# Performance work log

Measured on AMD Instinct MI355X. Metric: run time of the kernel, lower is better.

The kernel has to match this reference:

```python
import jax, jax.numpy as jnp
import numpy as np
import math
from jax import lax

B, T, IN_DIM, D, H, L, OUT = 2, 2048, 128, 512, 8, 4, 128
HD = D // H
FF = int(4.0 * D)
NEG = -1e30  # stands in for -inf in the causal mask (identical softmax result)


def setup_inputs() -> dict:
    key = jax.random.key(0)
    ks = jax.random.split(key, 8)
    s = 0.02
    def p(k, shape):
        return jax.random.normal(k, shape, jnp.float32) * s
    return {
        "x": jax.random.normal(ks[0], (B, T, IN_DIM), jnp.float32),
        "Win": p(ks[1], (IN_DIM, D)), "bin_": jnp.zeros((D,), jnp.float32),
        "Wqkv": p(ks[2], (L, D, 3 * D)), "bqkv": jnp.zeros((L, 3 * D), jnp.float32),
        "Wo": p(ks[3], (L, D, D)), "bo": jnp.zeros((L, D), jnp.float32),
        "ln1_g": jnp.ones((L, D), jnp.float32), "ln1_b": jnp.zeros((L, D), jnp.float32),
        "Wf1": p(ks[4], (L, D, FF)), "bf1": jnp.zeros((L, FF), jnp.float32),
        "Wf2": p(ks[5], (L, FF, D)), "bf2": jnp.zeros((L, D), jnp.float32),
        "ln2_g": jnp.ones((L, D), jnp.float32), "ln2_b": jnp.zeros((L, D), jnp.float32),
        "lnf_g": jnp.ones((D,), jnp.float32), "lnf_b": jnp.zeros((D,), jnp.float32),
        "Wout": p(ks[6], (D, OUT)), "bout": jnp.zeros((OUT,), jnp.float32),
    }


def _layernorm(x, g, b, eps=1e-5):
    mu = jnp.mean(x, axis=-1, keepdims=True)
    var = jnp.mean(jnp.square(x - mu), axis=-1, keepdims=True)
    return (x - mu) * lax.rsqrt(var + eps) * g + b


def _sinusoidal_pe(t, d):
    pos = jnp.arange(t, dtype=jnp.float32)[:, None]
    div = jnp.exp(jnp.arange(0, d, 2, dtype=jnp.float32) * (-math.log(10000.0) / d))
    pe = jnp.zeros((t, d), jnp.float32)
    pe = pe.at[:, 0::2].set(jnp.sin(pos * div)).at[:, 1::2].set(jnp.cos(pos * div))
    return pe


def _alibi_bias():
    # ALiBi slopes (H=8 is a power of 2): start = 2**(-2**(-(log2(H)-3)))
    start = 2.0 ** (-(2.0 ** (-(math.log2(H) - 3.0))))
    slopes = jnp.array([start * (start ** i) for i in range(H)], jnp.float32)
    pos = jnp.arange(T)
    dist = jnp.triu(pos[None, :] - pos[:, None]).astype(jnp.float32)  # faithful: .triu() zeroes j<i
    bias = slopes[:, None, None] * dist  # [H,T,T]
    causal = jnp.triu(jnp.ones((T, T), bool), 1)
    return jnp.where(causal[None], NEG, bias)


def _forward(x, Win, bin_, Wqkv, bqkv, Wo, bo, ln1_g, ln1_b, Wf1, bf1, Wf2, bf2,
             ln2_g, ln2_b, lnf_g, lnf_b, Wout, bout):
    x = x @ Win + bin_                      # [B,T,D] project_in
    x = x + _sinusoidal_pe(T, D)            # internal time embedding
    bias = _alibi_bias()                    # [H,T,T]
    scale = 1.0 / math.sqrt(HD)

    def block(h, params):
        wqkv, bq, wo, bo_, g1, b1, wf1, bf1_, wf2, bf2_, g2, b2 = params
        y = _layernorm(h, g1, b1)
        qkv = y @ wqkv + bq                 # [B,T,3D]
        q, k, v = jnp.split(qkv, 3, axis=-1)
        def heads(t):
            return t.reshape(B, T, H, HD).transpose(0, 2, 1, 3)  # [B,H,T,HD]
        q, k, v = heads(q), heads(k), heads(v)
        logits = jnp.einsum('bhqd,bhkd->bhqk', q, k) * scale + bias[None]
        attn = jax.nn.softmax(logits, axis=-1)
        y = jnp.einsum('bhqk,bhkd->bhqd', attn, v)
        y = y.transpose(0, 2, 1, 3).reshape(B, T, D)
        h = h + (y @ wo + bo_)
        y = _layernorm(h, g2, b2)
        y = jax.nn.gelu(y @ wf1 + bf1_, approximate=False) @ wf2 + bf2_
        h = h + y
        return h, None

    x, _ = lax.scan(block, x, (Wqkv, bqkv, Wo, bo, ln1_g, ln1_b, Wf1, bf1, Wf2, bf2, ln2_g, ln2_b))
    x = _layernorm(x, lnf_g, lnf_b)         # final_norm
    return x @ Wout + bout                  # output head


def reference(x, Win, bin_, Wqkv, bqkv, Wo, bo, ln1_g, ln1_b, Wf1, bf1, Wf2, bf2,
              ln2_g, ln2_b, lnf_g, lnf_b, Wout, bout):
    return _forward(x, Win, bin_, Wqkv, bqkv, Wo, bo, ln1_g, ln1_b, Wf1, bf1,
                    Wf2, bf2, ln2_g, ln2_b, lnf_g, lnf_b, Wout, bout)
```

## Files before the change

kernel.cpp:

```cpp
#include <hip/hip_runtime.h>
#include <math.h>
#include <type_traits>
#include <utility>

#define TT 2048
typedef unsigned short u16;
typedef unsigned int u32;
typedef float f32x4 __attribute__((ext_vector_type(4)));
typedef float f32x16 __attribute__((ext_vector_type(16)));
typedef short s16x8 __attribute__((ext_vector_type(8)));
typedef __bf16 bf16x8 __attribute__((ext_vector_type(8)));
typedef __bf16 bf16x2 __attribute__((ext_vector_type(2)));
typedef u32 u32x4 __attribute__((ext_vector_type(4)));

enum { EPI_PE = 0, EPI_QKV = 1, EPI_RES = 2, EPI_GELU = 3, EPI_OUTF = 4 };

template<typename V, typename = void> struct mfma_takes : std::false_type {};
template<typename V> struct mfma_takes<V, std::void_t<decltype(
    __builtin_amdgcn_mfma_f32_16x16x32_bf16(std::declval<V>(), std::declval<V>(),
                                            std::declval<f32x4>(), 0, 0, 0))>>
    : std::true_type {};

template<typename VA>
__device__ __forceinline__ f32x4 MFMA_t(VA a, VA b, f32x4 c) {
    if constexpr (mfma_takes<VA>::value) {
        return __builtin_amdgcn_mfma_f32_16x16x32_bf16(a, b, c, 0, 0, 0);
    } else {
        return __builtin_amdgcn_mfma_f32_16x16x32_bf16(
            __builtin_bit_cast(bf16x8, a), __builtin_bit_cast(bf16x8, b), c, 0, 0, 0);
    }
}

template<typename V, typename = void> struct mfma32_takes : std::false_type {};
template<typename V> struct mfma32_takes<V, std::void_t<decltype(
    __builtin_amdgcn_mfma_f32_32x32x16_bf16(std::declval<V>(), std::declval<V>(),
                                            std::declval<f32x16>(), 0, 0, 0))>>
    : std::true_type {};

template<typename VA>
__device__ __forceinline__ f32x16 MFMA32(VA a, VA b, f32x16 c) {
    if constexpr (mfma32_takes<VA>::value) {
        return __builtin_amdgcn_mfma_f32_32x32x16_bf16(a, b, c, 0, 0, 0);
    } else {
        return __builtin_amdgcn_mfma_f32_32x32x16_bf16(
            __builtin_bit_cast(bf16x8, a), __builtin_bit_cast(bf16x8, b), c, 0, 0, 0);
    }
}

__device__ __forceinline__ u16 f2b(float f) {
    u32 u = __float_as_uint(f);
    return (u16)((u + 0x7FFFu + ((u >> 16) & 1u)) >> 16);
}

__device__ __forceinline__ u32 pkbf(float a, float b) {
    bf16x2 t; t[0] = (__bf16)a; t[1] = (__bf16)b;
    return __builtin_bit_cast(u32, t);
}

__device__ __forceinline__ void gload16(const void* g, void* lds_base, int lds_byte_off) {
    __builtin_amdgcn_global_load_lds(
        (const __attribute__((address_space(1))) void*)g,
        (__attribute__((address_space(3))) void*)((char*)lds_base + lds_byte_off),
        16, 0, 0);
}

template<int EPI, int TM, int TN>
__global__ __launch_bounds__(256)
void k_gemm_mfma(const u16* __restrict__ A, const u16* __restrict__ Bt,
                 const float* __restrict__ bias, const float* __restrict__ Rf,
                 void* __restrict__ Cout, u16* __restrict__ Kfp,
                 u16* __restrict__ Vfp, int M, int N, int K)
{
    constexpr int MF = TM / 32;
    constexpr int NF = TN / 32;
    __shared__ __attribute__((aligned(16))) u16 SMEM[TM * 64 + TN * 64];
    u16* As = SMEM;
    u16* Bs = SMEM + TM * 64;
    const int tid = threadIdx.x;
    const int l = tid & 63, wv = tid >> 6;
    const int l15 = l & 15, lg = l >> 4;
    const int wr = wv >> 1, wc = wv & 1;
    const int row0 = blockIdx.y * TM, col0 = blockIdx.x * TN;

    f32x4 acc[MF][NF];
#pragma unroll
    for (int m = 0; m < MF; ++m)
#pragma unroll
        for (int n = 0; n < NF; ++n) acc[m][n] = (f32x4){0.f, 0.f, 0.f, 0.f};

    for (int kt = 0; kt < K; kt += 64) {
#pragma unroll
        for (int i = 0; i < TM / 32; ++i) {
            const int u = i * 256 + wv * 64 + l;
            const int ar = u >> 3, ac = u & 7;
            const int sc = (ac ^ (ar & 7)) << 3;
            const int off = __builtin_amdgcn_readfirstlane((i * 256 + wv * 64) * 16);
            gload16(A + (size_t)(row0 + ar) * K + kt + sc, As, off);
        }
#pragma unroll
        for (int i = 0; i < TN / 32; ++i) {
            const int u = i * 256 + wv * 64 + l;
            const int ar = u >> 3, ac = u & 7;
            const int sc = (ac ^ (ar & 7)) << 3;
            const int off = __builtin_amdgcn_readfirstlane((i * 256 + wv * 64) * 16);
            gload16(Bt + (size_t)(col0 + ar) * K + kt + sc, Bs, off);
        }
        __syncthreads();
        s16x8 af[MF][2], bf[NF][2];
#pragma unroll
        for (int m = 0; m < MF; ++m) {
            const int r = wr * (TM / 2) + m * 16 + l15;
#pragma unroll
            for (int s = 0; s < 2; ++s)
                af[m][s] = *(const s16x8*)(As + r * 64 + (((s * 4 + lg) ^ (r & 7)) << 3));
        }
#pragma unroll
        for (int n = 0; n < NF; ++n) {
            const int r = wc * (TN / 2) + n * 16 + l15;
#pragma unroll
            for (int s = 0; s < 2; ++s)
                bf[n][s] = *(const s16x8*)(Bs + r * 64 + (((s * 4 + lg) ^ (r & 7)) << 3));
        }
#pragma unroll
        for (int s = 0; s < 2; ++s)
#pragma unroll
            for (int m = 0; m < MF; ++m)
#pragma unroll
                for (int n = 0; n < NF; ++n)
                    acc[m][n] = MFMA_t(af[m][s], bf[n][s], acc[m][n]);
        __syncthreads();
    }

    if constexpr (EPI == EPI_QKV) {
        if (col0 < 512) {
#pragma unroll
            for (int m = 0; m < MF; ++m)
#pragma unroll
                for (int rg = 0; rg < 4; ++rg) {
                    const int row = row0 + wr * (TM / 2) + m * 16 + lg * 4 + rg;
#pragma unroll
                    for (int n = 0; n < NF; ++n) {
                        const int col = col0 + wc * (TN / 2) + n * 16 + l15;
                        ((u16*)Cout)[(size_t)row * N + col] = f2b(acc[m][n][rg] + bias[col]);
                    }
                }
        } else if (col0 < 1024) {
#pragma unroll
            for (int m = 0; m < MF; ++m)
#pragma unroll
                for (int rg = 0; rg < 4; ++rg) {
                    const int row = row0 + wr * (TM / 2) + m * 16 + lg * 4 + rg;
                    const int t = row & (TT - 1), bb = row >> 11;
#pragma unroll
                    for (int n = 0; n < NF; ++n) {
                        const int col = col0 + wc * (TN / 2) + n * 16 + l15;
                        const int dd = col - 512;
                        const int hh = dd >> 6, c = (dd >> 3) & 7, j = dd & 7;
                        Kfp[(((size_t)(bb * 8 + hh) * 8 + c) * 2048 + t) * 8 + j]
                            = f2b(acc[m][n][rg] + bias[col]);
                    }
                }
        } else {
            u16* TV = SMEM;
#pragma unroll
            for (int m = 0; m < MF; ++m)
#pragma unroll
                for (int rg = 0; rg < 4; ++rg) {
                    const int rr = wr * (TM / 2) + m * 16 + lg * 4 + rg;
#pragma unroll
                    for (int n = 0; n < NF; ++n) {
                        const int cc_ = wc * (TN / 2) + n * 16 + l15;
                        TV[rr * 128 + cc_] = f2b(acc[m][n][rg] + bias[col0 + cc_]);
                    }
                }
            __syncthreads();
            const int gt = (row0 & (TT - 1)) >> 6, bb = row0 >> 11;
            const int hh0 = (col0 - 1024) >> 6;
#pragma unroll
            for (int i = 0; i < 4; ++i) {
                const int u = i * 256 + tid;
                const int hsel = u >> 9, rem = u & 511;
                const int cc = rem >> 6, d = rem & 63;
                u32 pk[4];
#pragma unroll
                for (int jp = 0; jp < 4; ++jp)
                    pk[jp] = (u32)TV[(cc * 8 + 2 * jp) * 128 + hsel * 64 + d]
                           | ((u32)TV[(cc * 8 + 2 * jp + 1) * 128 + hsel * 64 + d] << 16);
                *(uint4*)(Vfp + ((((size_t)(bb * 8 + hh0 + hsel) * 32 + gt) * 8 + cc) * 64 + d) * 8)
                    = make_uint4(pk[0], pk[1], pk[2], pk[3]);
            }
        }
        return;
    }

#pragma unroll
    for (int m = 0; m < MF; ++m)
#pragma unroll
        for (int rg = 0; rg < 4; ++rg) {
            const int row = row0 + wr * (TM / 2) + m * 16 + lg * 4 + rg;
#pragma unroll
            for (int n = 0; n < NF; ++n) {
                const int col = col0 + wc * (TN / 2) + n * 16 + l15;
                float v = acc[m][n][rg] + bias[col];
                const size_t idx = (size_t)row * N + col;
                if constexpr (EPI == EPI_PE) {
                    const int t = row & (TT - 1);
                    const float freq = __expf(-(float)(col & ~1) * 0.017988946039015984f);
                    const float ang = (float)t * freq;
                    v += (col & 1) ? cosf(ang) : sinf(ang);
                    ((float*)Cout)[idx] = v;
                } else if constexpr (EPI == EPI_GELU) {
                    v = 0.5f * v * (1.f + erff(v * 0.7071067811865475f));
                    ((u16*)Cout)[idx] = f2b(v);
                } else if constexpr (EPI == EPI_RES) {
                    ((float*)Cout)[idx] = Rf[idx] + v;
                } else {
                    ((float*)Cout)[idx] = v;
                }
            }
        }
}

__global__ __launch_bounds__(256)
void k_ln(const float* __restrict__ X, const float* __restrict__ g,
          const float* __restrict__ b, u16* __restrict__ Y)
{
    const int lane = threadIdx.x & 63;
    const int row = blockIdx.x * 4 + (threadIdx.x >> 6);
    const float* x = X + (size_t)row * 512 + lane * 8;

    float4 v0 = *(const float4*)x;
    float4 v1 = *(const float4*)(x + 4);
    float vals[8] = {v0.x, v0.y, v0.z, v0.w, v1.x, v1.y, v1.z, v1.w};

    float s = 0.f;
#pragma unroll
    for (int i = 0; i < 8; ++i) s += vals[i];
#pragma unroll
    for (int off = 32; off >= 1; off >>= 1) s += __shfl_xor(s, off);
    const float mu = s * (1.f / 512.f);

    float sq = 0.f;
#pragma unroll
    for (int i = 0; i < 8; ++i) { float d = vals[i] - mu; sq += d * d; }
#pragma unroll
    for (int off = 32; off >= 1; off >>= 1) sq += __shfl_xor(sq, off);
    const float rs = rsqrtf(sq * (1.f / 512.f) + 1e-5f);

    const float* gp = g + lane * 8;
    const float* bp = b + lane * 8;
    float4 g0 = *(const float4*)gp, g1 = *(const float4*)(gp + 4);
    float4 b0 = *(const float4*)bp, b1 = *(const float4*)(bp + 4);
    float ga[8] = {g0.x, g0.y, g0.z, g0.w, g1.x, g1.y, g1.z, g1.w};
    float bb[8] = {b0.x, b0.y, b0.z, b0.w, b1.x, b1.y, b1.z, b1.w};

    u32 pk[4];
#pragma unroll
    for (int i = 0; i < 4; ++i) {
        float a0 = (vals[2 * i]     - mu) * rs * ga[2 * i]     + bb[2 * i];
        float a1 = (vals[2 * i + 1] - mu) * rs * ga[2 * i + 1] + bb[2 * i + 1];
        pk[i] = (u32)f2b(a0) | ((u32)f2b(a1) << 16);
    }
    *(uint4*)(Y + (size_t)row * 512 + lane * 8) = make_uint4(pk[0], pk[1], pk[2], pk[3]);
}

__global__ __launch_bounds__(256, 4)
void k_attn(const u16* __restrict__ qkv, const u16* __restrict__ Kf,
            const u16* __restrict__ Vf, u16* __restrict__ y)
{
    __shared__ float Om[4][32 * 65];
    __shared__ float Ml[4][32][2];
    const int tid = threadIdx.x;
    const int l = tid & 63, w = tid >> 6;
    const int l31 = l & 31, hi = l >> 5;
    const int bx = blockIdx.x;
    const int xcd = bx & 7, s = bx >> 3;
    const int bh = xcd * 2 + (s & 1);
    const int t_tile = 63 - (s >> 1);
    const int b = bh >> 3, hh = bh & 7;
    const int bT = b * TT, hh64 = hh * 64;

    const int qg = t_tile * 32 + l31;
    const int NT = (t_tile >> 1) + 1;

    f32x16 o[2] = {};
    float m = -1e30f, lsum = 0.f;

    if (w < NT) {
        s16x8 qf[4];
        {
            const u16* qsrc = qkv + (size_t)(bT + qg) * 1536 + hh64 + hi * 8;
#pragma unroll
            for (int dk = 0; dk < 4; ++dk) qf[dk] = *(const s16x8*)(qsrc + dk * 16);
        }
        const u16* kfb = Kf + ((size_t)bh * 8 + hi) * 2048 * 8;
        const u16* vfb = Vf + (((size_t)bh * 32) * 8 + hi) * 64 * 8;

        for (int g = w; g < NT; g += 4) {
            s16x8 kf[8];
#pragma unroll
            for (int nb = 0; nb < 2; ++nb)
#pragma unroll
                for (int dk = 0; dk < 4; ++dk)
                    kf[nb * 4 + dk] = *(const s16x8*)(
                        kfb + ((size_t)(dk * 2) * 2048 + g * 64 + nb * 32 + l31) * 8);

            f32x16 sA[2];
#pragma unroll
            for (int nb = 0; nb < 2; ++nb) {
                f32x16 acc = {};
#pragma unroll
                for (int dk = 0; dk < 4; ++dk) acc = MFMA32(kf[nb * 4 + dk], qf[dk], acc);
                sA[nb] = acc;
            }

            if (g == NT - 1) {
                const int kvb = g * 64, hi4 = hi * 4;
#pragma unroll
                for (int nb = 0; nb < 2; ++nb)
#pragma unroll
                    for (int r = 0; r < 16; ++r) {
                        const int kv = kvb + nb * 32 + (r & 3) + 8 * (r >> 2) + hi4;
                        sA[nb][r] = (kv > qg) ? -1e30f : sA[nb][r];
                    }
            }

            float tmp[16];
#pragma unroll
            for (int r = 0; r < 16; ++r) tmp[r] = fmaxf(sA[0][r], sA[1][r]);
#pragma unroll
            for (int st = 8; st >= 1; st >>= 1)
#pragma unroll
                for (int r = 0; r < 8; ++r)
                    if (r < st) tmp[r] = fmaxf(tmp[r], tmp[r + st]);
            float mt = fmaxf(tmp[0], __shfl_xor(tmp[0], 32));
            const bool grow = !__all(mt <= m);
            if (grow) {
                const float mn = fmaxf(m, mt);
                const float alpha = __expf((m - mn) * 0.125f);
                m = mn;
                lsum *= alpha;
#pragma unroll
                for (int dt = 0; dt < 2; ++dt)
#pragma unroll
                    for (int r = 0; r < 16; ++r) o[dt][r] *= alpha;
            }
            const float mc = -m * 0.125f;

            float p[2][16];
            float sum[16];
#pragma unroll
            for (int r = 0; r < 16; ++r) {
                p[0][r] = __expf(fmaf(sA[0][r], 0.125f, mc));
                p[1][r] = __expf(fmaf(sA[1][r], 0.125f, mc));
                sum[r] = p[0][r] + p[1][r];
            }
#pragma unroll
            for (int st = 8; st >= 1; st >>= 1)
#pragma unroll
                for (int r = 0; r < 8; ++r)
                    if (r < st) sum[r] += sum[r + st];
            float psum = sum[0] + __shfl_xor(sum[0], 32);
            lsum += psum;

            u32 pk2[2][8], sw2[2][8];
#pragma unroll
            for (int nb = 0; nb < 2; ++nb)
#pragma unroll
                for (int i = 0; i < 8; ++i) {
                    pk2[nb][i] = pkbf(p[nb][2 * i], p[nb][2 * i + 1]);
                    sw2[nb][i] = __shfl_xor(pk2[nb][i], 32);
                }
            s16x8 pa[4];
#pragma unroll
            for (int nb = 0; nb < 2; ++nb)
#pragma unroll
                for (int k16 = 0; k16 < 2; ++k16) {
                    const int i0 = k16 * 4;
                    u32 w0 = hi ? sw2[nb][i0 + 2] : pk2[nb][i0 + 0];
                    u32 w1 = hi ? sw2[nb][i0 + 3] : pk2[nb][i0 + 1];
                    u32 w2 = hi ? pk2[nb][i0 + 2] : sw2[nb][i0 + 0];
                    u32 w3 = hi ? pk2[nb][i0 + 3] : sw2[nb][i0 + 1];
                    u32x4 t4 = {w0, w1, w2, w3};
                    pa[nb * 2 + k16] = __builtin_bit_cast(s16x8, t4);
                }

#pragma unroll
            for (int dt = 0; dt < 2; ++dt) {
                f32x16 acc = o[dt];
#pragma unroll
                for (int ks = 0; ks < 4; ++ks)
                    acc = MFMA32(*(const s16x8*)(
                        vfb + (((size_t)g * 8 + ks * 2) * 64 + dt * 32 + l31) * 8),
                        pa[ks], acc);
                o[dt] = acc;
            }
        }
    }

#pragma unroll
    for (int dt = 0; dt < 2; ++dt)
#pragma unroll
        for (int r = 0; r < 16; ++r) {
            const int d = dt * 32 + (r & 3) + 8 * (r >> 2) + 4 * hi;
            Om[w][l31 * 65 + d] = o[dt][r];
        }
    Ml[w][l31][0] = m;
    Ml[w][l31][1] = lsum;
    __syncthreads();

    const int q = tid & 31, d0 = (tid >> 5) * 8;
    float m0 = Ml[0][q][0], m1 = Ml[1][q][0], m2 = Ml[2][q][0], m3 = Ml[3][q][0];
    const float mstar = fmaxf(fmaxf(m0, m1), fmaxf(m2, m3));
    float sc[4];
    sc[0] = __expf((m0 - mstar) * 0.125f);
    sc[1] = __expf((m1 - mstar) * 0.125f);
    sc[2] = __expf((m2 - mstar) * 0.125f);
    sc[3] = __expf((m3 - mstar) * 0.125f);
    const float lstar = sc[0] * Ml[0][q][1] + sc[1] * Ml[1][q][1]
                      + sc[2] * Ml[2][q][1] + sc[3] * Ml[3][q][1];
    float ov[8];
#pragma unroll
    for (int j = 0; j < 8; ++j) ov[j] = 0.f;
#pragma unroll
    for (int ww = 0; ww < 4; ++ww) {
        const float scw = sc[ww];
        const float* src = &Om[ww][q * 65 + d0];
#pragma unroll
        for (int j = 0; j < 8; ++j) ov[j] = fmaf(scw, src[j], ov[j]);
    }
    const float inv = 1.f / lstar;
    u32 pk[4];
#pragma unroll
    for (int i = 0; i < 4; ++i) pk[i] = pkbf(ov[2 * i] * inv, ov[2 * i + 1] * inv);
    u16* yp = y + (size_t)(bT + t_tile * 32 + q) * 512 + hh64 + d0;
    *(uint4*)yp = make_uint4(pk[0], pk[1], pk[2], pk[3]);
}

__global__ __launch_bounds__(256)
void k_wt_all(const float* __restrict__ Wqkv, const float* __restrict__ Wo,
              const float* __restrict__ Wf1, const float* __restrict__ Wf2,
              const float* __restrict__ Win, const float* __restrict__ Wout,
              u16* __restrict__ WqkvT, u16* __restrict__ WoT,
              u16* __restrict__ Wf1T, u16* __restrict__ Wf2T,
              u16* __restrict__ WinT, u16* __restrict__ WoutT)
{
    __shared__ float T[64][65];
    const int tid = threadIdx.x;
    int id = blockIdx.x;
    const float* W; u16* Wt; int K, N;
    if (id < 3072) {
        const int lyr = id / 768, sub = id - lyr * 768;
        if (sub < 192)      { W = Wqkv + (size_t)lyr * 512 * 1536; Wt = WqkvT + (size_t)lyr * 512 * 1536; K = 512;  N = 1536; id = sub; }
        else if (sub < 256) { W = Wo   + (size_t)lyr * 512 * 512;  Wt = WoT   + (size_t)lyr * 512 * 512;  K = 512;  N = 512;  id = sub - 192; }
        else if (sub < 512) { W = Wf1  + (size_t)lyr * 512 * 2048; Wt = Wf1T  + (size_t)lyr * 512 * 2048; K = 512;  N = 2048; id = sub - 256; }
        else                { W = Wf2  + (size_t)lyr * 2048 * 512; Wt = Wf2T  + (size_t)lyr * 2048 * 512; K = 2048; N = 512;  id = sub - 512; }
    } else if (id < 3088)   { W = Win;  Wt = WinT;  K = 128; N = 512; id -= 3072; }
    else                    { W = Wout; Wt = WoutT; K = 512; N = 128; id -= 3088; }
    const int nt = N >> 6;
    const int ktile = id / nt, ntile = id - ktile * nt;
    const int kb = ktile * 64, nb = ntile * 64;
#pragma unroll
    for (int i = 0; i < 4; ++i) {
        const int r = i * 16 + (tid >> 4), c = (tid & 15) * 4;
        const float4 v = *(const float4*)&W[(size_t)(kb + r) * N + nb + c];
        T[r][c] = v.x; T[r][c + 1] = v.y; T[r][c + 2] = v.z; T[r][c + 3] = v.w;
    }
    __syncthreads();
    const int n = tid >> 2, k0 = (tid & 3) * 16;
    u32 pk[8];
#pragma unroll
    for (int i = 0; i < 8; ++i)
        pk[i] = pkbf(T[k0 + 2 * i][n], T[k0 + 2 * i + 1][n]);
    uint4* dst = (uint4*)(Wt + (size_t)(nb + n) * K + kb + k0);
    dst[0] = make_uint4(pk[0], pk[1], pk[2], pk[3]);
    dst[1] = make_uint4(pk[4], pk[5], pk[6], pk[7]);
}

__global__ __launch_bounds__(256)
void k_f2b(const float* __restrict__ x, u16* __restrict__ xb)
{
    const int g = blockIdx.x * 256 + threadIdx.x;
    const float4* s = (const float4*)(x + (size_t)g * 8);
    float4 a = s[0], c = s[1];
    u32 pk[4] = {
        (u32)f2b(a.x) | ((u32)f2b(a.y) << 16), (u32)f2b(a.z) | ((u32)f2b(a.w) << 16),
        (u32)f2b(c.x) | ((u32)f2b(c.y) << 16), (u32)f2b(c.z) | ((u32)f2b(c.w) << 16)};
    *(uint4*)(xb + (size_t)g * 8) = make_uint4(pk[0], pk[1], pk[2], pk[3]);
}

extern "C" void kernel_launch(void* const* d_in, const int* in_sizes, int n_in,
                              void* d_out, int out_size, void* d_ws, size_t ws_size,
                              hipStream_t stream)
{
    const float* x    = (const float*)d_in[0];
    const float* Win  = (const float*)d_in[1];
    const float* bin_ = (const float*)d_in[2];
    const float* Wqkv = (const float*)d_in[3];
    const float* bqkv = (const float*)d_in[4];
    const float* Wo   = (const float*)d_in[5];
    const float* bo   = (const float*)d_in[6];
    const float* ln1g = (const float*)d_in[7];
    const float* ln1b = (const float*)d_in[8];
    const float* Wf1  = (const float*)d_in[9];
    const float* bf1  = (const float*)d_in[10];
    const float* Wf2  = (const float*)d_in[11];
    const float* bf2  = (const float*)d_in[12];
    const float* ln2g = (const float*)d_in[13];
    const float* ln2b = (const float*)d_in[14];
    const float* lnfg = (const float*)d_in[15];
    const float* lnfb = (const float*)d_in[16];
    const float* Wout = (const float*)d_in[17];
    const float* bout = (const float*)d_in[18];
    float* out = (float*)d_out;

    const int M = 4096;
    char* ws = (char*)d_ws;
    float* h    = (float*)(ws + 0);
    u16*   y    = (u16*)(ws + 8388608);
    u16*   big  = (u16*)(ws + 12582912);
    u16*   Kf   = (u16*)(ws + 29360128);
    u16*   Vf   = (u16*)(ws + 33554432);
    u16*   xb   = big;
    u16*   WinT  = (u16*)(ws + 37748736);
    u16*   WoutT = (u16*)(ws + 37879808);
    u16*   WqkvT = (u16*)(ws + 38010880);
    u16*   WoT   = (u16*)(ws + 44302336);
    u16*   Wf1T  = (u16*)(ws + 46399488);
    u16*   Wf2T  = (u16*)(ws + 54788096);

    dim3 blk(256);

    k_f2b<<<256, blk, 0, stream>>>(x, xb);
    k_wt_all<<<3104, blk, 0, stream>>>(Wqkv, Wo, Wf1, Wf2, Win, Wout,
                                       WqkvT, WoT, Wf1T, Wf2T, WinT, WoutT);

    k_gemm_mfma<EPI_PE, 64, 64><<<dim3(8, 64), blk, 0, stream>>>(
        xb, WinT, bin_, nullptr, h, nullptr, nullptr, M, 512, 128);

    for (int lyr = 0; lyr < 4; ++lyr) {
        k_ln<<<1024, blk, 0, stream>>>(h, ln1g + lyr * 512, ln1b + lyr * 512, y);
        k_gemm_mfma<EPI_QKV, 64, 128><<<dim3(12, 64), blk, 0, stream>>>(
            y, WqkvT + (size_t)lyr * 512 * 1536, bqkv + lyr * 1536, nullptr,
            big, Kf, Vf, M, 1536, 512);
        k_attn<<<1024, blk, 0, stream>>>(big, Kf, Vf, y);
        k_gemm_mfma<EPI_RES, 64, 64><<<dim3(8, 64), blk, 0, stream>>>(
            y, WoT + (size_t)lyr * 512 * 512, bo + lyr * 512, h, h, nullptr, nullptr, M, 512, 512);
        k_ln<<<1024, blk, 0, stream>>>(h, ln2g + lyr * 512, ln2b + lyr * 512, y);
        k_gemm_mfma<EPI_GELU, 64, 128><<<dim3(16, 64), blk, 0, stream>>>(
            y, Wf1T + (size_t)lyr * 512 * 2048, bf1 + lyr * 2048, nullptr,
            big, nullptr, nullptr, M, 2048, 512);
        k_gemm_mfma<EPI_RES, 64, 64><<<dim3(8, 64), blk, 0, stream>>>(
            big, Wf2T + (size_t)lyr * 2048 * 512, bf2 + lyr * 512, h, h, nullptr, nullptr, M, 512, 2048);
    }

    k_ln<<<1024, blk, 0, stream>>>(h, lnfg, lnfb, y);
    k_gemm_mfma<EPI_OUTF, 64, 64><<<dim3(2, 64), blk, 0, stream>>>(
        y, WoutT, bout, nullptr, out, nullptr, nullptr, M, 128, 512);
}
```

Measured before the change: 468.9 us.

## Switch GEMM to 32x32 MFMA, use exp2 in softmax, add setprio around MFMAs

The GEMM kernel now issues 32x32x16 bf16 MFMA instead of 16x16x32. Each wave computes 32-row fragments and reads four k-slices per 64-wide tile, and all epilogues are remapped to the 32x32 output layout. The attention kernel replaces __expf with the native exp2 by folding log2(e)/8 into the scale. It also raises wave priority around its MFMA blocks to favour matrix issue. This cuts operand-load and instruction overhead and exp cost, but it needs tiles that are multiples of 64 per wave and a correct remap of the output layout.

```diff
diff --git a/kernel.cpp b/kernel.cpp
--- a/kernel.cpp
+++ b/kernel.cpp
@@ -13,23 +13,10 @@
 typedef __bf16 bf16x2 __attribute__((ext_vector_type(2)));
 typedef u32 u32x4 __attribute__((ext_vector_type(4)));
 
+#define L2E8 0.1803368801111731f
+#define EXP2(x) __builtin_amdgcn_exp2f(x)
+
 enum { EPI_PE = 0, EPI_QKV = 1, EPI_RES = 2, EPI_GELU = 3, EPI_OUTF = 4 };
-
-template<typename V, typename = void> struct mfma_takes : std::false_type {};
-template<typename V> struct mfma_takes<V, std::void_t<decltype(
-    __builtin_amdgcn_mfma_f32_16x16x32_bf16(std::declval<V>(), std::declval<V>(),
-                                            std::declval<f32x4>(), 0, 0, 0))>>
-    : std::true_type {};
-
-template<typename VA>
-__device__ __forceinline__ f32x4 MFMA_t(VA a, VA b, f32x4 c) {
-    if constexpr (mfma_takes<VA>::value) {
-        return __builtin_amdgcn_mfma_f32_16x16x32_bf16(a, b, c, 0, 0, 0);
-    } else {
-        return __builtin_amdgcn_mfma_f32_16x16x32_bf16(
-            __builtin_bit_cast(bf16x8, a), __builtin_bit_cast(bf16x8, b), c, 0, 0, 0);
-    }
-}
 
 template<typename V, typename = void> struct mfma32_takes : std::false_type {};
 template<typename V> struct mfma32_takes<V, std::void_t<decltype(
@@ -71,22 +58,18 @@
                  void* __restrict__ Cout, u16* __restrict__ Kfp,
                  u16* __restrict__ Vfp, int M, int N, int K)
 {
-    constexpr int MF = TM / 32;
-    constexpr int NF = TN / 32;
+    constexpr int MF = TM / 64;
+    constexpr int NF = TN / 64;
     __shared__ __attribute__((aligned(16))) u16 SMEM[TM * 64 + TN * 64];
     u16* As = SMEM;
     u16* Bs = SMEM + TM * 64;
     const int tid = threadIdx.x;
     const int l = tid & 63, wv = tid >> 6;
-    const int l15 = l & 15, lg = l >> 4;
+    const int l31 = l & 31, hi = l >> 5;
     const int wr = wv >> 1, wc = wv & 1;
     const int row0 = blockIdx.y * TM, col0 = blockIdx.x * TN;
 
-    f32x4 acc[MF][NF];
-#pragma unroll
-    for (int m = 0; m < MF; ++m)
-#pragma unroll
-        for (int n = 0; n < NF; ++n) acc[m][n] = (f32x4){0.f, 0.f, 0.f, 0.f};
+    f32x16 acc[MF][NF] = {};
 
     for (int kt = 0; kt < K; kt += 64) {
 #pragma unroll
@@ -106,28 +89,28 @@
             gload16(Bt + (size_t)(col0 + ar) * K + kt + sc, Bs, off);
         }
         __syncthreads();
-        s16x8 af[MF][2], bf[NF][2];
+        s16x8 af[MF][4], bf[NF][4];
 #pragma unroll
         for (int m = 0; m < MF; ++m) {
-            const int r = wr * (TM / 2) + m * 16 + l15;
-#pragma unroll
-            for (int s = 0; s < 2; ++s)
-                af[m][s] = *(const s16x8*)(As + r * 64 + (((s * 4 + lg) ^ (r & 7)) << 3));
+            const int r = wr * (TM / 2) + m * 32 + l31;
+#pragma unroll
+            for (int kk = 0; kk < 4; ++kk)
+                af[m][kk] = *(const s16x8*)(As + r * 64 + (((kk * 2 + hi) ^ (r & 7)) << 3));
         }
 #pragma unroll
         for (int n = 0; n < NF; ++n) {
-            const int r = wc * (TN / 2) + n * 16 + l15;
-#pragma unroll
-            for (int s = 0; s < 2; ++s)
-                bf[n][s] = *(const s16x8*)(Bs + r * 64 + (((s * 4 + lg) ^ (r & 7)) << 3));
-        }
-#pragma unroll
-        for (int s = 0; s < 2; ++s)
+            const int r = wc * (TN / 2) + n * 32 + l31;
+#pragma unroll
+            for (int kk = 0; kk < 4; ++kk)
+                bf[n][kk] = *(const s16x8*)(Bs + r * 64 + (((kk * 2 + hi) ^ (r & 7)) << 3));
+        }
+#pragma unroll
+        for (int kk = 0; kk < 4; ++kk)
 #pragma unroll
             for (int m = 0; m < MF; ++m)
 #pragma unroll
                 for (int n = 0; n < NF; ++n)
-                    acc[m][n] = MFMA_t(af[m][s], bf[n][s], acc[m][n]);
+                    acc[m][n] = MFMA32(af[m][kk], bf[n][kk], acc[m][n]);
         __syncthreads();
     }
 
@@ -136,28 +119,28 @@
 #pragma unroll
             for (int m = 0; m < MF; ++m)
 #pragma unroll
-                for (int rg = 0; rg < 4; ++rg) {
-                    const int row = row0 + wr * (TM / 2) + m * 16 + lg * 4 + rg;
+                for (int r = 0; r < 16; ++r) {
+                    const int row = row0 + wr * (TM / 2) + m * 32 + (r & 3) + 8 * (r >> 2) + 4 * hi;
 #pragma unroll
                     for (int n = 0; n < NF; ++n) {
-                        const int col = col0 + wc * (TN / 2) + n * 16 + l15;
-                        ((u16*)Cout)[(size_t)row * N + col] = f2b(acc[m][n][rg] + bias[col]);
+                        const int col = col0 + wc * (TN / 2) + n * 32 + l31;
+                        ((u16*)Cout)[(size_t)row * N + col] = f2b(acc[m][n][r] + bias[col]);
                     }
                 }
         } else if (col0 < 1024) {
 #pragma unroll
             for (int m = 0; m < MF; ++m)
 #pragma unroll
-                for (int rg = 0; rg < 4; ++rg) {
-                    const int row = row0 + wr * (TM / 2) + m * 16 + lg * 4 + rg;
+                for (int r = 0; r < 16; ++r) {
+                    const int row = row0 + wr * (TM / 2) + m * 32 + (r & 3) + 8 * (r >> 2) + 4 * hi;
                     const int t = row & (TT - 1), bb = row >> 11;
 #pragma unroll
                     for (int n = 0; n < NF; ++n) {
-                        const int col = col0 + wc * (TN / 2) + n * 16 + l15;
+                        const int col = col0 + wc * (TN / 2) + n * 32 + l31;
                         const int dd = col - 512;
                         const int hh = dd >> 6, c = (dd >> 3) & 7, j = dd & 7;
                         Kfp[(((size_t)(bb * 8 + hh) * 8 + c) * 2048 + t) * 8 + j]
-                            = f2b(acc[m][n][rg] + bias[col]);
+                            = f2b(acc[m][n][r] + bias[col]);
                     }
                 }
         } else {
@@ -165,12 +148,12 @@
 #pragma unroll
             for (int m = 0; m < MF; ++m)
 #pragma unroll
-                for (int rg = 0; rg < 4; ++rg) {
-                    const int rr = wr * (TM / 2) + m * 16 + lg * 4 + rg;
+                for (int r = 0; r < 16; ++r) {
+                    const int rr = wr * (TM / 2) + m * 32 + (r & 3) + 8 * (r >> 2) + 4 * hi;
 #pragma unroll
                     for (int n = 0; n < NF; ++n) {
-                        const int cc_ = wc * (TN / 2) + n * 16 + l15;
-                        TV[rr * 128 + cc_] = f2b(acc[m][n][rg] + bias[col0 + cc_]);
+                        const int cc_ = wc * (TN / 2) + n * 32 + l31;
+                        TV[rr * 128 + cc_] = f2b(acc[m][n][r] + bias[col0 + cc_]);
                     }
                 }
             __syncthreads();
@@ -196,12 +179,12 @@
 #pragma unroll
     for (int m = 0; m < MF; ++m)
 #pragma unroll
-        for (int rg = 0; rg < 4; ++rg) {
-            const int row = row0 + wr * (TM / 2) + m * 16 + lg * 4 + rg;
+        for (int r = 0; r < 16; ++r) {
+            const int row = row0 + wr * (TM / 2) + m * 32 + (r & 3) + 8 * (r >> 2) + 4 * hi;
 #pragma unroll
             for (int n = 0; n < NF; ++n) {
-                const int col = col0 + wc * (TN / 2) + n * 16 + l15;
-                float v = acc[m][n][rg] + bias[col];
+                const int col = col0 + wc * (TN / 2) + n * 32 + l31;
+                float v = acc[m][n][r] + bias[col];
                 const size_t idx = (size_t)row * N + col;
                 if constexpr (EPI == EPI_PE) {
                     const int t = row & (TT - 1);
@@ -306,6 +289,7 @@
                         kfb + ((size_t)(dk * 2) * 2048 + g * 64 + nb * 32 + l31) * 8);
 
             f32x16 sA[2];
+            __builtin_amdgcn_s_setprio(1);
 #pragma unroll
             for (int nb = 0; nb < 2; ++nb) {
                 f32x16 acc = {};
@@ -313,6 +297,7 @@
                 for (int dk = 0; dk < 4; ++dk) acc = MFMA32(kf[nb * 4 + dk], qf[dk], acc);
                 sA[nb] = acc;
             }
+            __builtin_amdgcn_s_setprio(0);
 
             if (g == NT - 1) {
                 const int kvb = g * 64, hi4 = hi * 4;
@@ -337,7 +322,7 @@
             const bool grow = !__all(mt <= m);
             if (grow) {
                 const float mn = fmaxf(m, mt);
-                const float alpha = __expf((m - mn) * 0.125f);
+                const float alpha = EXP2((m - mn) * L2E8);
                 m = mn;
                 lsum *= alpha;
 #pragma unroll
@@ -345,14 +330,14 @@
 #pragma unroll
                     for (int r = 0; r < 16; ++r) o[dt][r] *= alpha;
             }
-            const float mc = -m * 0.125f;
+            const float mc = -m * L2E8;
 
             float p[2][16];
             float sum[16];
 #pragma unroll
             for (int r = 0; r < 16; ++r) {
-                p[0][r] = __expf(fmaf(sA[0][r], 0.125f, mc));
-                p[1][r] = __expf(fmaf(sA[1][r], 0.125f, mc));
+                p[0][r] = EXP2(fmaf(sA[0][r], L2E8, mc));
+                p[1][r] = EXP2(fmaf(sA[1][r], L2E8, mc));
                 sum[r] = p[0][r] + p[1][r];
             }
 #pragma unroll
@@ -385,6 +370,7 @@
                     pa[nb * 2 + k16] = __builtin_bit_cast(s16x8, t4);
                 }
 
+            __builtin_amdgcn_s_setprio(1);
 #pragma unroll
             for (int dt = 0; dt < 2; ++dt) {
                 f32x16 acc = o[dt];
@@ -395,6 +381,7 @@
                         pa[ks], acc);
                 o[dt] = acc;
             }
+            __builtin_amdgcn_s_setprio(0);
         }
     }
 
@@ -413,10 +400,10 @@
     float m0 = Ml[0][q][0], m1 = Ml[1][q][0], m2 = Ml[2][q][0], m3 = Ml[3][q][0];
     const float mstar = fmaxf(fmaxf(m0, m1), fmaxf(m2, m3));
     float sc[4];
-    sc[0] = __expf((m0 - mstar) * 0.125f);
-    sc[1] = __expf((m1 - mstar) * 0.125f);
-    sc[2] = __expf((m2 - mstar) * 0.125f);
-    sc[3] = __expf((m3 - mstar) * 0.125f);
+    sc[0] = EXP2((m0 - mstar) * L2E8);
+    sc[1] = EXP2((m1 - mstar) * L2E8);
+    sc[2] = EXP2((m2 - mstar) * L2E8);
+    sc[3] = EXP2((m3 - mstar) * L2E8);
     const float lstar = sc[0] * Ml[0][q][1] + sc[1] * Ml[1][q][1]
                       + sc[2] * Ml[2][q][1] + sc[3] * Ml[3][q][1];
     float ov[8];
```

New measurement: 434.9 us, median of 2. 1.08x faster.
